# Performance work log

Hardware: AMD Instinct MI355X
Metric: run time of the kernel (lower is better)

## Reference

```python
import jax, jax.numpy as jnp
import numpy as np

HEADS = 16
DIM_HEAD = 64
SCALE = DIM_HEAD ** -0.5


def setup_inputs() -> dict:
    key = jax.random.key(0)
    k1, k2, k3 = jax.random.split(key, 3)
    B, N, C = 2, 2048, 1024
    inner = HEADS * DIM_HEAD  # 1024
    x = jax.random.normal(k1, (B, N, C), dtype=jnp.float32)
    w_qkv = jax.random.normal(k2, (C, 3 * inner), dtype=jnp.float32) * (C ** -0.5)
    w_proj = jax.random.normal(k3, (inner, C), dtype=jnp.float32) * (inner ** -0.5)
    b_proj = jnp.zeros((C,), dtype=jnp.float32)
    return {"x": x, "w_qkv": w_qkv, "w_proj": w_proj, "b_proj": b_proj}


def reference(x, w_qkv, w_proj, b_proj):
    B, N, C = x.shape
    qkv = x @ w_qkv  # [B, N, 3*inner]
    qkv = qkv.reshape(B, N, 3, HEADS, DIM_HEAD)
    qkv = jnp.transpose(qkv, (2, 0, 3, 1, 4))  # [3, B, H, N, D]
    q, k, v = qkv[0], qkv[1], qkv[2]
    q = q * SCALE
    attn = jnp.einsum('bhnd,bhmd->bhnm', q, k)  # [B, H, N, N]
    attn = jax.nn.softmax(attn, axis=-1)
    out = jnp.einsum('bhnm,bhmd->bhnd', attn, v)  # [B, H, N, D]
    out = jnp.transpose(out, (0, 2, 1, 3)).reshape(B, N, HEADS * DIM_HEAD)
    return out @ w_proj + b_proj
```

## Files before the change

kernel.cpp:

```cpp
#include <hip/hip_runtime.h>
#include <hip/hip_bf16.h>
#include <cstdint>
#include <cstddef>

static constexpr int BATCH = 2;
static constexpr int SEQ   = 2048;
static constexpr int CDIM  = 1024;
static constexpr int ROWS  = BATCH * SEQ;
static constexpr int QKVN  = 3 * CDIM;

typedef short bf16x8 __attribute__((ext_vector_type(8)));
typedef short bf16x4 __attribute__((ext_vector_type(4)));
typedef float f32x4  __attribute__((ext_vector_type(4)));

__device__ inline short f2bf(float f) {
    union { float f; unsigned u; } v; v.f = f;
    unsigned u = v.u;
    u += 0x7fffu + ((u >> 16) & 1u);
    return (short)(u >> 16);
}

__device__ inline unsigned pk_bf16(float a, float b) {
    union { float f; unsigned u; } ua, ub;
    ua.f = a; ub.f = b;
    unsigned xa = ua.u + 0x7fffu + ((ua.u >> 16) & 1u);
    unsigned xb = ub.u + 0x7fffu + ((ub.u >> 16) & 1u);
    return __builtin_amdgcn_perm(xb, xa, 0x07060302);
}

__device__ inline void glds16(const short* g, short* l) {
    __builtin_amdgcn_global_load_lds(
        (const __attribute__((address_space(1))) void*)g,
        (__attribute__((address_space(3))) void*)l, 16, 0, 0);
}

__device__ inline f32x4 mfma16_bf16(bf16x4 a, bf16x4 b, f32x4 c) {
#if __has_builtin(__builtin_amdgcn_mfma_f32_16x16x16bf16_1k)
    return __builtin_amdgcn_mfma_f32_16x16x16bf16_1k(a, b, c, 0, 0, 0);
#else
    asm("v_mfma_f32_16x16x16_bf16 %0, %1, %2, %0" : "+v"(c) : "v"(a), "v"(b));
    return c;
#endif
}

__global__ __launch_bounds__(256) void cvt_f32_bf16(const float* __restrict__ in,
                                                    short* __restrict__ out, int n4) {
    int i = blockIdx.x * 256 + threadIdx.x;
    if (i >= n4) return;
    float4 f = ((const float4*)in)[i];
    uint2 o;
    o.x = pk_bf16(f.x, f.y);
    o.y = pk_bf16(f.z, f.w);
    ((uint2*)out)[i] = o;
}

__global__ __launch_bounds__(256) void cvt_transpose(const float* __restrict__ in,
                                                     short* __restrict__ out, int R, int C,
                                                     float scale, int srows) {
    __shared__ float tile[32][33];
    int tx = threadIdx.x & 31, ty = threadIdx.x >> 5;
    int r0 = blockIdx.y * 32, c0 = blockIdx.x * 32;
    #pragma unroll
    for (int i = 0; i < 4; i++)
        tile[ty + i * 8][tx] = in[(size_t)(r0 + ty + i * 8) * C + c0 + tx];
    __syncthreads();
    #pragma unroll
    for (int i = 0; i < 4; i++) {
        int orow = c0 + ty + i * 8;
        float sc = (orow < srows) ? scale : 1.0f;
        out[(size_t)orow * R + r0 + tx] = f2bf(tile[tx][ty + i * 8] * sc);
    }
}

__global__ __launch_bounds__(256) void v_transpose(const short* __restrict__ qkv,
                                                   short* __restrict__ vTg) {
    __shared__ short tile[32][33];
    int bh = blockIdx.z, b = bh >> 4, h = bh & 15;
    int n0 = blockIdx.x * 32, d0 = blockIdx.y * 32;
    int tx = threadIdx.x & 31, ty = threadIdx.x >> 5;
    const short* src = qkv + (size_t)(b * SEQ) * QKVN + 2048 + h * 64;
    #pragma unroll
    for (int i = 0; i < 4; i++)
        tile[ty + i * 8][tx] = src[(size_t)(n0 + ty + i * 8) * QKVN + d0 + tx];
    __syncthreads();
    short* dst = vTg + (size_t)bh * (64 * SEQ);
    #pragma unroll
    for (int i = 0; i < 4; i++)
        dst[(size_t)(d0 + ty + i * 8) * SEQ + n0 + tx] = tile[tx][ty + i * 8];
}

template<int BF16OUT, int MT>
__global__ __launch_bounds__(256) void gemm_bt(const short* __restrict__ A,
                                               const short* __restrict__ Bt,
                                               void* __restrict__ C,
                                               const float* __restrict__ bias,
                                               int M, int N, int K) {
    constexpr int AF = MT / 32;
    __shared__ __align__(16) short As[MT * 32];
    __shared__ __align__(16) short Bs[128 * 32];

    const int t = threadIdx.x, wave = t >> 6, lane = t & 63;
    const int l15 = lane & 15, quad = lane >> 4;
    const int wr = wave >> 1, wc = wave & 1;
    const int m0 = blockIdx.y * MT, n0 = blockIdx.x * 128;

    f32x4 acc[AF][4] = {};

    const short* gA = A  + (size_t)(m0 + wave * (MT / 4) + (lane >> 2)) * K + (lane & 3) * 8;
    const short* gB = Bt + (size_t)(n0 + wave * 32 + (lane >> 2)) * K + (lane & 3) * 8;
    short* lA = &As[wave * (MT / 4) * 32];
    short* lB = &Bs[wave * 32 * 32];

    for (int k0 = 0; k0 < K; k0 += 32) {
        glds16(gA + k0, lA);
        if constexpr (MT == 128) glds16(gA + 16 * K + k0, lA + 512);
        glds16(gB + k0,          lB);
        glds16(gB + 16 * K + k0, lB + 512);
        __syncthreads();

        bf16x8 af[AF], bf[4];
        #pragma unroll
        for (int i = 0; i < AF; i++)
            af[i] = *(const bf16x8*)&As[(wr * (MT / 2) + i * 16 + l15) * 32 + quad * 8];
        #pragma unroll
        for (int j = 0; j < 4; j++)
            bf[j] = *(const bf16x8*)&Bs[(wc * 64 + j * 16 + l15) * 32 + quad * 8];
        #pragma unroll
        for (int i = 0; i < AF; i++)
            #pragma unroll
            for (int j = 0; j < 4; j++)
                acc[i][j] = __builtin_amdgcn_mfma_f32_16x16x32_bf16(af[i], bf[j], acc[i][j], 0, 0, 0);
        __syncthreads();
    }

    #pragma unroll
    for (int i = 0; i < AF; i++) {
        #pragma unroll
        for (int j = 0; j < 4; j++) {
            #pragma unroll
            for (int r = 0; r < 4; r++) {
                int row = m0 + wr * (MT / 2) + i * 16 + quad * 4 + r;
                int col = n0 + wc * 64 + j * 16 + l15;
                float v = acc[i][j][r];
                if (BF16OUT) ((short*)C)[(size_t)row * N + col] = f2bf(v);
                else         ((float*)C)[(size_t)row * N + col] = v + bias[col];
            }
        }
    }
}

static constexpr int KP      = 128 * 32;
static constexpr int VT_OFF  = 2 * KP;
static constexpr int LDV     = 136;
static constexpr int SMEM_SH = VT_OFF + 64 * LDV;

__global__ __launch_bounds__(256) void attn_kernel(const short* __restrict__ qkv,
                                                   const short* __restrict__ vTg,
                                                   short* __restrict__ attn_out) {
    __shared__ __align__(16) short smem[SMEM_SH];

    const int t = threadIdx.x, wave = t >> 6, lane = t & 63;
    const int l15 = lane & 15, quad = lane >> 4;
    const int bh = blockIdx.y, b = bh >> 4, h = bh & 15;
    const int q0 = blockIdx.x * 64;
    const size_t baseQ = (size_t)(b * SEQ) * QKVN + h * 64;

    const size_t qoff = baseQ + (size_t)(q0 + wave * 16 + l15) * QKVN + quad * 8;
    bf16x8 qf0 = *(const bf16x8*)&qkv[qoff];
    bf16x8 qf1 = *(const bf16x8*)&qkv[qoff + 32];

    const short* gK = qkv + baseQ + 1024
                    + (size_t)(wave * 32 + (lane >> 2)) * QKVN + (lane & 3) * 8;
    short* lK0 = smem + wave * 1024;
    short* lK1 = smem + KP + wave * 1024;

    const short* gV = vTg + (size_t)bh * (64 * SEQ);
    const int vd = t >> 3, vc = t & 7;

    const bf16x4 ones = { (short)0x3F80, (short)0x3F80, (short)0x3F80, (short)0x3F80 };

    float m_i = -INFINITY;
    f32x4 ot[4] = {};
    f32x4 ol = {};

    for (int j0 = 0; j0 < SEQ; j0 += 128) {
        const size_t jadd = (size_t)j0 * QKVN;
        glds16(gK + jadd,                       lK0);
        glds16(gK + jadd + (size_t)16 * QKVN,   lK0 + 512);
        glds16(gK + jadd + 32,                  lK1);
        glds16(gK + jadd + (size_t)16 * QKVN + 32, lK1 + 512);
        {
            int4 v00 = *(const int4*)&gV[(size_t)vd * SEQ + j0 + vc * 8];
            int4 v01 = *(const int4*)&gV[(size_t)vd * SEQ + j0 + 64 + vc * 8];
            int4 v10 = *(const int4*)&gV[(size_t)(vd + 32) * SEQ + j0 + vc * 8];
            int4 v11 = *(const int4*)&gV[(size_t)(vd + 32) * SEQ + j0 + 64 + vc * 8];
            *(int4*)&smem[VT_OFF + vd * LDV + vc * 8]             = v00;
            *(int4*)&smem[VT_OFF + vd * LDV + 64 + vc * 8]        = v01;
            *(int4*)&smem[VT_OFF + (vd + 32) * LDV + vc * 8]      = v10;
            *(int4*)&smem[VT_OFF + (vd + 32) * LDV + 64 + vc * 8] = v11;
        }
        __syncthreads();

        f32x4 s[8];
        #pragma unroll
        for (int sub = 0; sub < 8; sub++) {
            bf16x8 kf0 = *(const bf16x8*)&smem[(sub * 16 + l15) * 32 + quad * 8];
            bf16x8 kf1 = *(const bf16x8*)&smem[KP + (sub * 16 + l15) * 32 + quad * 8];
            f32x4 a = {};
            a = __builtin_amdgcn_mfma_f32_16x16x32_bf16(kf0, qf0, a, 0, 0, 0);
            a = __builtin_amdgcn_mfma_f32_16x16x32_bf16(kf1, qf1, a, 0, 0, 0);
            s[sub] = a;
        }

        float m4[8];
        #pragma unroll
        for (int sub = 0; sub < 8; sub++)
            m4[sub] = fmaxf(fmaxf(s[sub][0], s[sub][1]), fmaxf(s[sub][2], s[sub][3]));
        float mx = fmaxf(fmaxf(fmaxf(m4[0], m4[1]), fmaxf(m4[2], m4[3])),
                         fmaxf(fmaxf(m4[4], m4[5]), fmaxf(m4[6], m4[7])));
        mx = fmaxf(mx, __shfl_xor(mx, 16));
        mx = fmaxf(mx, __shfl_xor(mx, 32));
        float mn = fmaxf(m_i, mx);
        if (!__all(mn == m_i)) {
            float alpha = __builtin_amdgcn_exp2f(m_i - mn);
            m_i = mn;
            #pragma unroll
            for (int r = 0; r < 4; r++) {
                ot[0][r] *= alpha; ot[1][r] *= alpha;
                ot[2][r] *= alpha; ot[3][r] *= alpha;
                ol[r]    *= alpha;
            }
        }

        #pragma unroll
        for (int sub = 0; sub < 8; sub++) {
            float p0 = __builtin_amdgcn_exp2f(s[sub][0] - m_i);
            float p1 = __builtin_amdgcn_exp2f(s[sub][1] - m_i);
            float p2 = __builtin_amdgcn_exp2f(s[sub][2] - m_i);
            float p3 = __builtin_amdgcn_exp2f(s[sub][3] - m_i);
            union { unsigned u[2]; bf16x4 v; } pu;
            pu.u[0] = pk_bf16(p0, p1);
            pu.u[1] = pk_bf16(p2, p3);
            ol = mfma16_bf16(ones, pu.v, ol);
            #pragma unroll
            for (int d = 0; d < 4; d++) {
                bf16x4 vf = *(const bf16x4*)&smem[VT_OFF + (d * 16 + l15) * LDV
                                                 + sub * 16 + quad * 4];
                ot[d] = mfma16_bf16(vf, pu.v, ot[d]);
            }
        }
        __syncthreads();
    }

    float inv = 1.0f / ol[0];
    #pragma unroll
    for (int d = 0; d < 4; d++) {
        unsigned w0 = pk_bf16(ot[d][0] * inv, ot[d][1] * inv);
        unsigned w1 = pk_bf16(ot[d][2] * inv, ot[d][3] * inv);
        *(unsigned*)&smem[VT_OFF + (wave * 16 + l15) * LDV + d * 16 + quad * 4]     = w0;
        *(unsigned*)&smem[VT_OFF + (wave * 16 + l15) * LDV + d * 16 + quad * 4 + 2] = w1;
    }
    __syncthreads();
    {
        int row = t >> 3, ch = t & 7;
        #pragma unroll
        for (int p = 0; p < 2; p++) {
            int rr = row + p * 32;
            int4 v = *(const int4*)&smem[VT_OFF + rr * LDV + ch * 8];
            *(int4*)&attn_out[(size_t)(b * SEQ + q0 + rr) * CDIM + h * 64 + ch * 8] = v;
        }
    }
}

extern "C" void kernel_launch(void* const* d_in, const int* in_sizes, int n_in,
                              void* d_out, int out_size, void* d_ws, size_t ws_size,
                              hipStream_t stream) {
    const float* x      = (const float*)d_in[0];
    const float* w_qkv  = (const float*)d_in[1];
    const float* w_proj = (const float*)d_in[2];
    const float* b_proj = (const float*)d_in[3];
    float* out = (float*)d_out;

    char* ws = (char*)d_ws;
    short* x_bf    = (short*)(ws);
    short* wqkvT   = (short*)(ws + 8388608);
    short* wprojT  = (short*)(ws + 14680064);
    short* qkv_bf  = (short*)(ws + 16777216);
    short* attn_bf = (short*)(ws + 41943040);
    short* vTg     = x_bf;

    const float SMUL = 0.125f * 1.44269504088896340736f;

    cvt_f32_bf16<<<4096, 256, 0, stream>>>(x, x_bf, ROWS * CDIM / 4);
    cvt_transpose<<<dim3(QKVN / 32, CDIM / 32), 256, 0, stream>>>(w_qkv, wqkvT, CDIM, QKVN,
                                                                  SMUL, 1024);
    cvt_transpose<<<dim3(CDIM / 32, CDIM / 32), 256, 0, stream>>>(w_proj, wprojT, CDIM, CDIM,
                                                                  1.0f, 0);

    gemm_bt<1, 128><<<dim3(QKVN / 128, ROWS / 128), 256, 0, stream>>>(
        x_bf, wqkvT, qkv_bf, nullptr, ROWS, QKVN, CDIM);

    v_transpose<<<dim3(SEQ / 32, 2, BATCH * 16), 256, 0, stream>>>(qkv_bf, vTg);

    attn_kernel<<<dim3(SEQ / 64, BATCH * 16), 256, 0, stream>>>(qkv_bf, vTg, attn_bf);

    gemm_bt<0, 64><<<dim3(CDIM / 128, ROWS / 64), 256, 0, stream>>>(
        attn_bf, wprojT, out, b_proj, ROWS, CDIM, CDIM);
}
```

Before: 216.5 us.

## Fuse prep kernels, compute V transposed via GEMM, widen attention blocks to 512 threads

The three conversion kernels are merged into one prep launch. The separate V-transpose pass is removed by computing V^T directly as a GEMM (W_v^T times x^T), with Q/K produced separately into a narrower buffer. The attention kernel now handles 128 queries per block with 8 waves, sharing each K/V tile across more waves and halving per-thread load work. pk_bf16 uses the hardware packed convert when available. Risks include lower attention occupancy from the 512-thread blocks and a V GEMM with a less favourable shape.

Result: no change. 212.8 us (-1.7%).

```diff
diff --git a/kernel.cpp b/kernel.cpp
--- a/kernel.cpp
+++ b/kernel.cpp
@@ -8,6 +8,7 @@
 static constexpr int CDIM  = 1024;
 static constexpr int ROWS  = BATCH * SEQ;
 static constexpr int QKVN  = 3 * CDIM;
+static constexpr int QKN   = 2 * CDIM;
 
 typedef short bf16x8 __attribute__((ext_vector_type(8)));
 typedef short bf16x4 __attribute__((ext_vector_type(4)));
@@ -21,11 +22,16 @@
 }
 
 __device__ inline unsigned pk_bf16(float a, float b) {
+#if __has_builtin(__builtin_amdgcn_cvt_pk_bf16_f32)
+    auto r = __builtin_amdgcn_cvt_pk_bf16_f32(a, b);
+    return __builtin_bit_cast(unsigned, r);
+#else
     union { float f; unsigned u; } ua, ub;
     ua.f = a; ub.f = b;
     unsigned xa = ua.u + 0x7fffu + ((ua.u >> 16) & 1u);
     unsigned xb = ub.u + 0x7fffu + ((ub.u >> 16) & 1u);
     return __builtin_amdgcn_perm(xb, xa, 0x07060302);
+#endif
 }
 
 __device__ inline void glds16(const short* g, short* l) {
@@ -43,23 +49,37 @@
 #endif
 }
 
-__global__ __launch_bounds__(256) void cvt_f32_bf16(const float* __restrict__ in,
-                                                    short* __restrict__ out, int n4) {
-    int i = blockIdx.x * 256 + threadIdx.x;
-    if (i >= n4) return;
-    float4 f = ((const float4*)in)[i];
-    uint2 o;
-    o.x = pk_bf16(f.x, f.y);
-    o.y = pk_bf16(f.z, f.w);
-    ((uint2*)out)[i] = o;
-}
-
-__global__ __launch_bounds__(256) void cvt_transpose(const float* __restrict__ in,
-                                                     short* __restrict__ out, int R, int C,
-                                                     float scale, int srows) {
+__global__ __launch_bounds__(256) void prep(const float* __restrict__ x,
+                                            const float* __restrict__ wqkv,
+                                            const float* __restrict__ wproj,
+                                            short* __restrict__ x_bf,
+                                            short* __restrict__ wqkvT,
+                                            short* __restrict__ wprojT,
+                                            float smul) {
     __shared__ float tile[32][33];
-    int tx = threadIdx.x & 31, ty = threadIdx.x >> 5;
-    int r0 = blockIdx.y * 32, c0 = blockIdx.x * 32;
+    const int bid = blockIdx.x, t = threadIdx.x;
+    if (bid < 4096) {
+        int i = bid * 256 + t;
+        float4 f = ((const float4*)x)[i];
+        uint2 o;
+        o.x = pk_bf16(f.x, f.y);
+        o.y = pk_bf16(f.z, f.w);
+        ((uint2*)x_bf)[i] = o;
+        return;
+    }
+    const float* in; short* out; int C, r0, c0; float scale; int srows;
+    if (bid < 7168) {
+        int b2 = bid - 4096;
+        in = wqkv; out = wqkvT; C = QKVN;
+        c0 = (b2 % 96) * 32; r0 = (b2 / 96) * 32;
+        scale = smul; srows = 1024;
+    } else {
+        int b3 = bid - 7168;
+        in = wproj; out = wprojT; C = CDIM;
+        c0 = (b3 & 31) * 32; r0 = (b3 >> 5) * 32;
+        scale = 1.0f; srows = 0;
+    }
+    int tx = t & 31, ty = t >> 5;
     #pragma unroll
     for (int i = 0; i < 4; i++)
         tile[ty + i * 8][tx] = in[(size_t)(r0 + ty + i * 8) * C + c0 + tx];
@@ -68,25 +88,8 @@
     for (int i = 0; i < 4; i++) {
         int orow = c0 + ty + i * 8;
         float sc = (orow < srows) ? scale : 1.0f;
-        out[(size_t)orow * R + r0 + tx] = f2bf(tile[tx][ty + i * 8] * sc);
-    }
-}
-
-__global__ __launch_bounds__(256) void v_transpose(const short* __restrict__ qkv,
-                                                   short* __restrict__ vTg) {
-    __shared__ short tile[32][33];
-    int bh = blockIdx.z, b = bh >> 4, h = bh & 15;
-    int n0 = blockIdx.x * 32, d0 = blockIdx.y * 32;
-    int tx = threadIdx.x & 31, ty = threadIdx.x >> 5;
-    const short* src = qkv + (size_t)(b * SEQ) * QKVN + 2048 + h * 64;
-    #pragma unroll
-    for (int i = 0; i < 4; i++)
-        tile[ty + i * 8][tx] = src[(size_t)(n0 + ty + i * 8) * QKVN + d0 + tx];
-    __syncthreads();
-    short* dst = vTg + (size_t)bh * (64 * SEQ);
-    #pragma unroll
-    for (int i = 0; i < 4; i++)
-        dst[(size_t)(d0 + ty + i * 8) * SEQ + n0 + tx] = tile[tx][ty + i * 8];
+        out[(size_t)orow * CDIM + r0 + tx] = f2bf(tile[tx][ty + i * 8] * sc);
+    }
 }
 
 template<int BF16OUT, int MT>
@@ -154,7 +157,7 @@
 static constexpr int LDV     = 136;
 static constexpr int SMEM_SH = VT_OFF + 64 * LDV;
 
-__global__ __launch_bounds__(256) void attn_kernel(const short* __restrict__ qkv,
+__global__ __launch_bounds__(512) void attn_kernel(const short* __restrict__ qk,
                                                    const short* __restrict__ vTg,
                                                    short* __restrict__ attn_out) {
     __shared__ __align__(16) short smem[SMEM_SH];
@@ -162,19 +165,19 @@
     const int t = threadIdx.x, wave = t >> 6, lane = t & 63;
     const int l15 = lane & 15, quad = lane >> 4;
     const int bh = blockIdx.y, b = bh >> 4, h = bh & 15;
-    const int q0 = blockIdx.x * 64;
-    const size_t baseQ = (size_t)(b * SEQ) * QKVN + h * 64;
-
-    const size_t qoff = baseQ + (size_t)(q0 + wave * 16 + l15) * QKVN + quad * 8;
-    bf16x8 qf0 = *(const bf16x8*)&qkv[qoff];
-    bf16x8 qf1 = *(const bf16x8*)&qkv[qoff + 32];
-
-    const short* gK = qkv + baseQ + 1024
-                    + (size_t)(wave * 32 + (lane >> 2)) * QKVN + (lane & 3) * 8;
-    short* lK0 = smem + wave * 1024;
-    short* lK1 = smem + KP + wave * 1024;
-
-    const short* gV = vTg + (size_t)bh * (64 * SEQ);
+    const int q0 = blockIdx.x * 128;
+    const size_t baseQ = (size_t)(b * SEQ) * QKN + h * 64;
+
+    const size_t qoff = baseQ + (size_t)(q0 + wave * 16 + l15) * QKN + quad * 8;
+    bf16x8 qf0 = *(const bf16x8*)&qk[qoff];
+    bf16x8 qf1 = *(const bf16x8*)&qk[qoff + 32];
+
+    const short* gK = qk + baseQ + 1024
+                    + (size_t)(wave * 16 + (lane >> 2)) * QKN + (lane & 3) * 8;
+    short* lK0 = smem + wave * 512;
+    short* lK1 = smem + KP + wave * 512;
+
+    const short* gV = vTg + (size_t)(h * 64) * ROWS + b * SEQ;
     const int vd = t >> 3, vc = t & 7;
 
     const bf16x4 ones = { (short)0x3F80, (short)0x3F80, (short)0x3F80, (short)0x3F80 };
@@ -184,20 +187,14 @@
     f32x4 ol = {};
 
     for (int j0 = 0; j0 < SEQ; j0 += 128) {
-        const size_t jadd = (size_t)j0 * QKVN;
-        glds16(gK + jadd,                       lK0);
-        glds16(gK + jadd + (size_t)16 * QKVN,   lK0 + 512);
-        glds16(gK + jadd + 32,                  lK1);
-        glds16(gK + jadd + (size_t)16 * QKVN + 32, lK1 + 512);
+        const size_t jadd = (size_t)j0 * QKN;
+        glds16(gK + jadd,      lK0);
+        glds16(gK + jadd + 32, lK1);
         {
-            int4 v00 = *(const int4*)&gV[(size_t)vd * SEQ + j0 + vc * 8];
-            int4 v01 = *(const int4*)&gV[(size_t)vd * SEQ + j0 + 64 + vc * 8];
-            int4 v10 = *(const int4*)&gV[(size_t)(vd + 32) * SEQ + j0 + vc * 8];
-            int4 v11 = *(const int4*)&gV[(size_t)(vd + 32) * SEQ + j0 + 64 + vc * 8];
-            *(int4*)&smem[VT_OFF + vd * LDV + vc * 8]             = v00;
-            *(int4*)&smem[VT_OFF + vd * LDV + 64 + vc * 8]        = v01;
-            *(int4*)&smem[VT_OFF + (vd + 32) * LDV + vc * 8]      = v10;
-            *(int4*)&smem[VT_OFF + (vd + 32) * LDV + 64 + vc * 8] = v11;
+            int4 v0 = *(const int4*)&gV[(size_t)vd * ROWS + j0 + vc * 8];
+            int4 v1 = *(const int4*)&gV[(size_t)vd * ROWS + j0 + 64 + vc * 8];
+            *(int4*)&smem[VT_OFF + vd * LDV + vc * 8]      = v0;
+            *(int4*)&smem[VT_OFF + vd * LDV + 64 + vc * 8] = v1;
         }
         __syncthreads();
 
@@ -257,16 +254,16 @@
     for (int d = 0; d < 4; d++) {
         unsigned w0 = pk_bf16(ot[d][0] * inv, ot[d][1] * inv);
         unsigned w1 = pk_bf16(ot[d][2] * inv, ot[d][3] * inv);
-        *(unsigned*)&smem[VT_OFF + (wave * 16 + l15) * LDV + d * 16 + quad * 4]     = w0;
-        *(unsigned*)&smem[VT_OFF + (wave * 16 + l15) * LDV + d * 16 + quad * 4 + 2] = w1;
+        *(unsigned*)&smem[(wave * 16 + l15) * 72 + d * 16 + quad * 4]     = w0;
+        *(unsigned*)&smem[(wave * 16 + l15) * 72 + d * 16 + quad * 4 + 2] = w1;
     }
     __syncthreads();
     {
         int row = t >> 3, ch = t & 7;
         #pragma unroll
         for (int p = 0; p < 2; p++) {
-            int rr = row + p * 32;
-            int4 v = *(const int4*)&smem[VT_OFF + rr * LDV + ch * 8];
+            int rr = row + p * 64;
+            int4 v = *(const int4*)&smem[rr * 72 + ch * 8];
             *(int4*)&attn_out[(size_t)(b * SEQ + q0 + rr) * CDIM + h * 64 + ch * 8] = v;
         }
     }
@@ -285,24 +282,21 @@
     short* x_bf    = (short*)(ws);
     short* wqkvT   = (short*)(ws + 8388608);
     short* wprojT  = (short*)(ws + 14680064);
-    short* qkv_bf  = (short*)(ws + 16777216);
+    short* qk_bf   = (short*)(ws + 16777216);
+    short* vTg     = (short*)(ws + 33554432);
     short* attn_bf = (short*)(ws + 41943040);
-    short* vTg     = x_bf;
 
     const float SMUL = 0.125f * 1.44269504088896340736f;
 
-    cvt_f32_bf16<<<4096, 256, 0, stream>>>(x, x_bf, ROWS * CDIM / 4);
-    cvt_transpose<<<dim3(QKVN / 32, CDIM / 32), 256, 0, stream>>>(w_qkv, wqkvT, CDIM, QKVN,
-                                                                  SMUL, 1024);
-    cvt_transpose<<<dim3(CDIM / 32, CDIM / 32), 256, 0, stream>>>(w_proj, wprojT, CDIM, CDIM,
-                                                                  1.0f, 0);
-
-    gemm_bt<1, 128><<<dim3(QKVN / 128, ROWS / 128), 256, 0, stream>>>(
-        x_bf, wqkvT, qkv_bf, nullptr, ROWS, QKVN, CDIM);
-
-    v_transpose<<<dim3(SEQ / 32, 2, BATCH * 16), 256, 0, stream>>>(qkv_bf, vTg);
-
-    attn_kernel<<<dim3(SEQ / 64, BATCH * 16), 256, 0, stream>>>(qkv_bf, vTg, attn_bf);
+    prep<<<8192, 256, 0, stream>>>(x, w_qkv, w_proj, x_bf, wqkvT, wprojT, SMUL);
+
+    gemm_bt<1, 128><<<dim3(QKN / 128, ROWS / 128), 256, 0, stream>>>(
+        x_bf, wqkvT, qk_bf, nullptr, ROWS, QKN, CDIM);
+
+    gemm_bt<1, 64><<<dim3(ROWS / 128, CDIM / 64), 256, 0, stream>>>(
+        wqkvT + (size_t)QKN * CDIM, x_bf, vTg, nullptr, CDIM, ROWS, CDIM);
+
+    attn_kernel<<<dim3(SEQ / 128, BATCH * 16), 512, 0, stream>>>(qk_bf, vTg, attn_bf);
 
     gemm_bt<0, 64><<<dim3(CDIM / 128, ROWS / 64), 256, 0, stream>>>(
         attn_bf, wprojT, out, b_proj, ROWS, CDIM, CDIM);
```
